# Performance work log

Hardware: AMD Instinct MI355X
Metric: run time of the kernel (lower is better)

Reference implementation:

```python
import jax, jax.numpy as jnp
import numpy as np

N, E, G = 100000, 1600000, 64
IN, H, OUT = 128, 64, 16  # hidden/2 = 32
SLOPE = 0.01


def setup_inputs() -> dict:
    key = jax.random.key(0)
    ks = jax.random.split(key, 7)
    features = jax.random.normal(ks[0], (N, IN), dtype=jnp.float32)
    src = jax.random.randint(ks[1], (E,), 0, N)
    dst = jax.random.randint(ks[2], (E,), 0, N)
    graph_ids = jnp.sort(jax.random.randint(ks[3], (N,), 0, G))
    # kaiming-uniform-ish fan_in init, bias=False everywhere
    W1 = jax.random.uniform(ks[4], (IN, H), jnp.float32, -1.0, 1.0) * np.sqrt(3.0 / IN)
    W2 = jax.random.uniform(ks[5], (H, H // 2), jnp.float32, -1.0, 1.0) * np.sqrt(3.0 / H)
    Wc = jax.random.uniform(ks[6], (H // 2, OUT), jnp.float32, -1.0, 1.0) * np.sqrt(3.0 / (H // 2))
    return {"features": features, "src": src, "dst": dst, "graph_ids": graph_ids,
            "W1": W1, "W2": W2, "Wc": Wc}


def _graph_conv(x, W, src, dst, n):
    # DGL GraphConv, norm='both', bias=False:
    # out = D_in^{-1/2} A (D_out^{-1/2} x) W   (degrees clamped to >= 1)
    ones = jnp.ones(src.shape[0], dtype=x.dtype)
    outdeg = jnp.clip(jax.ops.segment_sum(ones, src, num_segments=n), 1.0)
    indeg = jnp.clip(jax.ops.segment_sum(ones, dst, num_segments=n), 1.0)
    h = (x * jax.lax.rsqrt(outdeg)[:, None]) @ W  # project first (in_dim > out_dim)
    m = jax.ops.segment_sum(h[src], dst, num_segments=n)  # sparse aggregation
    return m * jax.lax.rsqrt(indeg)[:, None]


def reference(features, src, dst, graph_ids, W1, W2, Wc):
    h = jax.nn.leaky_relu(_graph_conv(features, W1, src, dst, N), SLOPE)
    h = jax.nn.leaky_relu(_graph_conv(h, W2, src, dst, N), SLOPE)
    # dropout is identity at inference
    sums = jax.ops.segment_sum(h, graph_ids, num_segments=G)
    cnts = jnp.clip(jax.ops.segment_sum(jnp.ones((N,), h.dtype), graph_ids, num_segments=G), 1.0)
    mean = sums / cnts[:, None]  # dgl.mean_nodes
    return mean @ Wc  # [G, OUT]
```

## Files before the change

### kernel.cpp

```cpp
#include <hip/hip_runtime.h>

#define NN 100000
#define NE 1600000
#define NG 64
#define D_IN 128
#define D_H 64
#define D_H2 32
#define D_OUT 16
#define SLOPE 0.01f
#define REC 48

#define BSH 9
#define NBK 196
#define NCB 500
#define CHE (NE / NCB)
#define PCAP 48

typedef _Float16 half2v __attribute__((ext_vector_type(2)));
typedef _Float16 h8 __attribute__((ext_vector_type(8)));
typedef float f32x4 __attribute__((ext_vector_type(4)));

__global__ __launch_bounds__(512) void p12_scatter(const int* __restrict__ src,
                                                   const int* __restrict__ dst,
                                                   unsigned* __restrict__ pkD,
                                                   unsigned short* __restrict__ pkS,
                                                   int* __restrict__ cntD,
                                                   int* __restrict__ cntS,
                                                   float* __restrict__ pool) {
  __shared__ unsigned stD[NBK][PCAP];
  __shared__ unsigned short stS[NBK][PCAP];
  __shared__ int cD[NBK], cS[NBK];
  int b = blockIdx.x, t = threadIdx.x;
  if (b == 0) {
    for (int i = t; i < NG * D_H2; i += 512) pool[i] = 0.f;
  }
  for (int i = t; i < NBK; i += 512) { cD[i] = 0; cS[i] = 0; }
  __syncthreads();
  const int4* s4 = (const int4*)(src + b * CHE);
  const int4* d4 = (const int4*)(dst + b * CHE);
  for (int i = t; i < CHE / 4; i += 512) {
    int4 s = s4[i], d = d4[i];
#pragma unroll
    for (int j = 0; j < 4; ++j) {
      int ss = (j == 0) ? s.x : (j == 1) ? s.y : (j == 2) ? s.z : s.w;
      int dd = (j == 0) ? d.x : (j == 1) ? d.y : (j == 2) ? d.z : d.w;
      int kd = dd >> BSH;
      int pd = atomicAdd(&cD[kd], 1);
      if (pd < PCAP) stD[kd][pd] = ((unsigned)(dd & 511) << 17) | (unsigned)ss;
      int ks = ss >> BSH;
      int ps = atomicAdd(&cS[ks], 1);
      if (ps < PCAP) stS[ks][ps] = (unsigned short)(ss & 511);
    }
  }
  __syncthreads();
  int wid = t >> 6, lane = t & 63;
  for (int k = wid; k < NBK; k += 8) {
    int cd = min(cD[k], PCAP), cs = min(cS[k], PCAP);
    if (lane < cd) pkD[((size_t)k * NCB + b) * PCAP + lane] = stD[k][lane];
    if (lane < cs) pkS[((size_t)k * NCB + b) * PCAP + lane] = stS[k][lane];
  }
  for (int i = t; i < NBK; i += 512) {
    cntD[i * NCB + b] = min(cD[i], PCAP);
    cntS[i * NCB + b] = min(cS[i], PCAP);
  }
}

__global__ __launch_bounds__(512) void p3_build(const unsigned* __restrict__ pkD,
                                                const unsigned short* __restrict__ pkS,
                                                const int* __restrict__ cntD,
                                                const int* __restrict__ cntS,
                                                int* __restrict__ adj,
                                                int* __restrict__ indeg,
                                                int* __restrict__ outdeg) {
  __shared__ int hh[512];
  int bb = blockIdx.x, t = threadIdx.x;
  hh[t] = 0;
  __syncthreads();
  if (bb < NBK) {
    int k = bb;
    int n0 = k << BSH;
    if (t < NCB) {
      int cnt = cntD[k * NCB + t];
      const uint4* r4 = (const uint4*)(pkD + ((size_t)k * NCB + t) * PCAP);
      for (int i = 0; i * 4 < cnt; ++i) {
        uint4 v = r4[i];
#pragma unroll
        for (int j = 0; j < 4; ++j) {
          int idx = i * 4 + j;
          if (idx < cnt) {
            unsigned rec = (j == 0) ? v.x : (j == 1) ? v.y : (j == 2) ? v.z : v.w;
            int local = rec >> 17;
            int pos = atomicAdd(&hh[local], 1);
            if (pos < REC) adj[(size_t)(n0 + local) * REC + pos] = (int)(rec & 0x1FFFF);
          }
        }
      }
    }
    __syncthreads();
    int n = n0 + t;
    if (n < NN) indeg[n] = hh[t];
  } else {
    int k = bb - NBK;
    if (t < NCB) {
      int cnt = cntS[k * NCB + t];
      const uint4* r4 = (const uint4*)(pkS + ((size_t)k * NCB + t) * PCAP);
      for (int i = 0; i * 8 < cnt; ++i) {
        uint4 v = r4[i];
        const unsigned short* u = (const unsigned short*)&v;
#pragma unroll
        for (int j = 0; j < 8; ++j) {
          int idx = i * 8 + j;
          if (idx < cnt) atomicAdd(&hh[u[j]], 1);
        }
      }
    }
    __syncthreads();
    int n0 = k << BSH;
    int n = n0 + t;
    if (n < NN) outdeg[n] = hh[t];
  }
}

__global__ __launch_bounds__(256) void k_mm1f(const float* __restrict__ X,
                                              const float* __restrict__ W,
                                              const int* __restrict__ odeg,
                                              _Float16* __restrict__ Y) {
  __shared__ _Float16 Wt[64][136];
  int t = threadIdx.x;
  if (blockIdx.x == 0 && t < 64) Y[(size_t)NN * 64 + t] = (_Float16)0.f;
  for (int i = t; i < 128 * 64; i += 256) {
    int k = i >> 6, f = i & 63;
    Wt[f][k] = (_Float16)W[i];
  }
  __syncthreads();
  int lane = t & 63, w = t >> 6;
  int m = lane & 15, q = lane >> 4;
  h8 bf[4][4];
#pragma unroll
  for (int kc = 0; kc < 4; ++kc)
#pragma unroll
    for (int nt = 0; nt < 4; ++nt)
      bf[kc][nt] = *(const h8*)&Wt[nt * 16 + m][kc * 32 + q * 8];

  const int NT = NN / 16;
  int idx = blockIdx.x * 4 + w;
  int t0 = idx * 2, t1 = t0 + 1;
  f32x4 r0[8], r1[8];
  if (t0 < NT) {
    const f32x4* X0 = (const f32x4*)(X + (size_t)(t0 * 16 + m) * 128);
#pragma unroll
    for (int kc = 0; kc < 4; ++kc) {
      r0[kc * 2 + 0] = X0[kc * 8 + q * 2 + 0];
      r0[kc * 2 + 1] = X0[kc * 8 + q * 2 + 1];
    }
  }
  if (t1 < NT) {
    const f32x4* X1 = (const f32x4*)(X + (size_t)(t1 * 16 + m) * 128);
#pragma unroll
    for (int kc = 0; kc < 4; ++kc) {
      r1[kc * 2 + 0] = X1[kc * 8 + q * 2 + 0];
      r1[kc * 2 + 1] = X1[kc * 8 + q * 2 + 1];
    }
  }
#pragma unroll
  for (int half = 0; half < 2; ++half) {
    int tile = (half == 0) ? t0 : t1;
    if (tile >= NT) continue;
    f32x4* rr = (half == 0) ? r0 : r1;
    f32x4 acc[4] = {{0,0,0,0},{0,0,0,0},{0,0,0,0},{0,0,0,0}};
#pragma unroll
    for (int kc = 0; kc < 4; ++kc) {
      f32x4 x0 = rr[kc * 2 + 0], x1 = rr[kc * 2 + 1];
      h8 a;
      a[0] = (_Float16)x0.x; a[1] = (_Float16)x0.y;
      a[2] = (_Float16)x0.z; a[3] = (_Float16)x0.w;
      a[4] = (_Float16)x1.x; a[5] = (_Float16)x1.y;
      a[6] = (_Float16)x1.z; a[7] = (_Float16)x1.w;
#pragma unroll
      for (int nt = 0; nt < 4; ++nt)
        acc[nt] = __builtin_amdgcn_mfma_f32_16x16x32_f16(a, bf[kc][nt], acc[nt], 0, 0, 0);
    }
    int n0 = tile * 16;
#pragma unroll
    for (int reg = 0; reg < 4; ++reg) {
      int nn = n0 + q * 4 + reg;
      float sc = rsqrtf((float)max(odeg[nn], 1));
#pragma unroll
      for (int nt = 0; nt < 4; ++nt)
        Y[(size_t)nn * 64 + nt * 16 + m] = (_Float16)(acc[nt][reg] * sc);
    }
  }
}

__global__ __launch_bounds__(128)
void k_aggmm2(const int* __restrict__ adj,
              const int* __restrict__ indeg,
              const int* __restrict__ odeg,
              const h8* __restrict__ H8,
              const float* __restrict__ W,
              _Float16* __restrict__ Y) {
  __shared__ int Adj[16][REC];
  __shared__ int Deg[16];
  __shared__ _Float16 Ht[16][72];
  __shared__ _Float16 Wt[32][72];
  int t = threadIdx.x;
  if (blockIdx.x == 0 && t < 32) Y[(size_t)NN * 32 + t] = (_Float16)0.f;
  for (int i = t; i < 64 * 32; i += 128) {
    int k = i >> 5, f = i & 31;
    Wt[f][k] = (_Float16)W[i];
  }
  int node0 = blockIdx.x * 16;
  {
    const int4* gadj = (const int4*)(adj + (size_t)node0 * REC);
    for (int i = t; i < 16 * (REC / 4); i += 128)
      ((int4*)Adj)[i] = gadj[i];
    if (t < 16) Deg[t] = indeg[node0 + t];
  }
  __syncthreads();
  for (int i = t; i < 16 * REC; i += 128) {
    int ndc = i / REC, j = i % REC;
    if (j >= min(Deg[ndc], REC)) Adj[ndc][j] = NN;
  }
  __syncthreads();
  int l8 = t & 7;
  int nd = t >> 3;
  int deg = Deg[nd];
  int groups = (min(deg, REC) + 15) >> 4;
  float acc[8] = {0.f, 0.f, 0.f, 0.f, 0.f, 0.f, 0.f, 0.f};
  for (int g = 0; g < groups; ++g) {
    int4 c0 = *(const int4*)&Adj[nd][g * 16 + 0];
    int4 c1 = *(const int4*)&Adj[nd][g * 16 + 4];
    int4 c2 = *(const int4*)&Adj[nd][g * 16 + 8];
    int4 c3 = *(const int4*)&Adj[nd][g * 16 + 12];
    h8 v0 = H8[(size_t)c0.x * 8 + l8];
    h8 v1 = H8[(size_t)c0.y * 8 + l8];
    h8 v2 = H8[(size_t)c0.z * 8 + l8];
    h8 v3 = H8[(size_t)c0.w * 8 + l8];
    h8 v4 = H8[(size_t)c1.x * 8 + l8];
    h8 v5 = H8[(size_t)c1.y * 8 + l8];
    h8 v6 = H8[(size_t)c1.z * 8 + l8];
    h8 v7 = H8[(size_t)c1.w * 8 + l8];
    h8 v8 = H8[(size_t)c2.x * 8 + l8];
    h8 v9 = H8[(size_t)c2.y * 8 + l8];
    h8 va = H8[(size_t)c2.z * 8 + l8];
    h8 vb = H8[(size_t)c2.w * 8 + l8];
    h8 vc = H8[(size_t)c3.x * 8 + l8];
    h8 vd = H8[(size_t)c3.y * 8 + l8];
    h8 ve = H8[(size_t)c3.z * 8 + l8];
    h8 vf = H8[(size_t)c3.w * 8 + l8];
#pragma unroll
    for (int j = 0; j < 8; ++j)
      acc[j] += ((((float)v0[j] + (float)v1[j]) + ((float)v2[j] + (float)v3[j])) +
                 (((float)v4[j] + (float)v5[j]) + ((float)v6[j] + (float)v7[j]))) +
                ((((float)v8[j] + (float)v9[j]) + ((float)va[j] + (float)vb[j])) +
                 (((float)vc[j] + (float)vd[j]) + ((float)ve[j] + (float)vf[j])));
  }
  float sc = rsqrtf((float)max(deg, 1));
  h8 hv;
#pragma unroll
  for (int j = 0; j < 8; ++j) {
    float x = acc[j] * sc;
    hv[j] = (_Float16)((x > 0.f) ? x : SLOPE * x);
  }
  *(h8*)&Ht[nd][l8 * 8] = hv;
  __syncthreads();
  int lane = t & 63, w = t >> 6;
  int m = lane & 15, q = lane >> 4;
  h8 bf[2], af[2];
#pragma unroll
  for (int kc = 0; kc < 2; ++kc) {
    bf[kc] = *(const h8*)&Wt[w * 16 + m][kc * 32 + q * 8];
    af[kc] = *(const h8*)&Ht[m][kc * 32 + q * 8];
  }
  f32x4 acc2 = {0, 0, 0, 0};
#pragma unroll
  for (int kc = 0; kc < 2; ++kc)
    acc2 = __builtin_amdgcn_mfma_f32_16x16x32_f16(af[kc], bf[kc], acc2, 0, 0, 0);
#pragma unroll
  for (int reg = 0; reg < 4; ++reg) {
    int nn = node0 + q * 4 + reg;
    float sco = rsqrtf((float)max(odeg[nn], 1));
    Y[(size_t)nn * 32 + w * 16 + m] = (_Float16)(acc2[reg] * sco);
  }
}

__global__ __launch_bounds__(128)
void k_agg32p(const int* __restrict__ adj,
              const int* __restrict__ indeg,
              const int* __restrict__ gid,
              const h8* __restrict__ H8,
              float* __restrict__ pool) {
  __shared__ int Adj2[32][REC];
  __shared__ int Deg2[32];
  __shared__ float lp[4][D_H2];
  __shared__ int gmin_s;
  int t = threadIdx.x;
  int l4 = t & 3;
  int nd = t >> 2;
  int node0 = blockIdx.x * 32;
  int node = node0 + nd;
  if (t == 0) gmin_s = gid[node0];
  if (t < 4 * D_H2) ((float*)lp)[t] = 0.f;
  {
    const int4* gadj = (const int4*)(adj + (size_t)node0 * REC);
    for (int i = t; i < 32 * (REC / 4); i += 128)
      ((int4*)Adj2)[i] = gadj[i];
    if (t < 32) Deg2[t] = indeg[node0 + t];
  }
  __syncthreads();
  for (int i = t; i < 32 * REC; i += 128) {
    int ndc = i / REC, j = i % REC;
    if (j >= min(Deg2[ndc], REC)) Adj2[ndc][j] = NN;
  }
  __syncthreads();
  int deg = Deg2[nd];
  int groups = (min(deg, REC) + 15) >> 4;
  float acc[8] = {0.f, 0.f, 0.f, 0.f, 0.f, 0.f, 0.f, 0.f};
  for (int g = 0; g < groups; ++g) {
    int4 c0 = *(const int4*)&Adj2[nd][g * 16 + 0];
    int4 c1 = *(const int4*)&Adj2[nd][g * 16 + 4];
    int4 c2 = *(const int4*)&Adj2[nd][g * 16 + 8];
    int4 c3 = *(const int4*)&Adj2[nd][g * 16 + 12];
    h8 v0 = H8[(size_t)c0.x * 4 + l4];
    h8 v1 = H8[(size_t)c0.y * 4 + l4];
    h8 v2 = H8[(size_t)c0.z * 4 + l4];
    h8 v3 = H8[(size_t)c0.w * 4 + l4];
    h8 v4 = H8[(size_t)c1.x * 4 + l4];
    h8 v5 = H8[(size_t)c1.y * 4 + l4];
    h8 v6 = H8[(size_t)c1.z * 4 + l4];
    h8 v7 = H8[(size_t)c1.w * 4 + l4];
    h8 v8 = H8[(size_t)c2.x * 4 + l4];
    h8 v9 = H8[(size_t)c2.y * 4 + l4];
    h8 va = H8[(size_t)c2.z * 4 + l4];
    h8 vb = H8[(size_t)c2.w * 4 + l4];
    h8 vc = H8[(size_t)c3.x * 4 + l4];
    h8 vd = H8[(size_t)c3.y * 4 + l4];
    h8 ve = H8[(size_t)c3.z * 4 + l4];
    h8 vf = H8[(size_t)c3.w * 4 + l4];
#pragma unroll
    for (int j = 0; j < 8; ++j)
      acc[j] += ((((float)v0[j] + (float)v1[j]) + ((float)v2[j] + (float)v3[j])) +
                 (((float)v4[j] + (float)v5[j]) + ((float)v6[j] + (float)v7[j]))) +
                ((((float)v8[j] + (float)v9[j]) + ((float)va[j] + (float)vb[j])) +
                 (((float)vc[j] + (float)vd[j]) + ((float)ve[j] + (float)vf[j])));
  }
  {
    float sc = rsqrtf((float)max(deg, 1));
    int gl = min(gid[node] - gmin_s, 3);
#pragma unroll
    for (int j = 0; j < 8; ++j) {
      float x = acc[j] * sc;
      x = (x > 0.f) ? x : SLOPE * x;
      atomicAdd(&lp[gl][l4 * 8 + j], x);
    }
  }
  __syncthreads();
  {
    float v = ((float*)lp)[t];
    if (v != 0.f) {
      int gl = t >> 5, f = t & 31;
      atomicAdd(&pool[(gmin_s + gl) * D_H2 + f], v);
    }
  }
}

__global__ __launch_bounds__(256) void k_out(const float* __restrict__ pool,
                                             const int* __restrict__ gid,
                                             const float* __restrict__ Wc,
                                             float* __restrict__ out) {
  __shared__ int bnd[NG + 1];
  __shared__ float mean[NG][D_H2];
  int t = threadIdx.x;
  if (t <= NG) {
    int target = t;
    int lo = 0, hi = NN;
    while (lo < hi) {
      int mid = (lo + hi) >> 1;
      if (gid[mid] < target) lo = mid + 1; else hi = mid;
    }
    bnd[t] = lo;
  }
  __syncthreads();
  for (int i = t; i < NG * D_H2; i += 256) {
    int g = i >> 5;
    float inv = 1.0f / (float)max(bnd[g + 1] - bnd[g], 1);
    ((float*)mean)[i] = pool[i] * inv;
  }
  __syncthreads();
  for (int i = t; i < NG * D_OUT; i += 256) {
    int g = i / D_OUT, o = i % D_OUT;
    float s = 0.f;
#pragma unroll
    for (int c = 0; c < D_H2; ++c) s += mean[g][c] * Wc[c * D_OUT + o];
    out[i] = s;
  }
}

extern "C" void kernel_launch(void* const* d_in, const int* in_sizes, int n_in,
                              void* d_out, int out_size, void* d_ws, size_t ws_size,
                              hipStream_t stream) {
  const float* X  = (const float*)d_in[0];
  const int*   src = (const int*)d_in[1];
  const int*   dst = (const int*)d_in[2];
  const int*   gid = (const int*)d_in[3];
  const float* W1 = (const float*)d_in[4];
  const float* W2 = (const float*)d_in[5];
  const float* Wc = (const float*)d_in[6];
  float* out = (float*)d_out;

  char* p = (char*)d_ws;
  auto alloc = [&](size_t bytes) {
    char* q = p;
    p += (bytes + 255) & ~(size_t)255;
    return q;
  };
  float*          pool   = (float*)alloc(NG * D_H2 * 4);
  int*            outdeg = (int*)alloc(NN * 4);
  int*            indeg  = (int*)alloc(NN * 4);
  int*            cntD   = (int*)alloc((size_t)NBK * NCB * 4);
  int*            cntS   = (int*)alloc((size_t)NBK * NCB * 4);
  unsigned*       pkD    = (unsigned*)alloc((size_t)NBK * NCB * PCAP * 4);
  unsigned short* pkS    = (unsigned short*)alloc((size_t)NBK * NCB * PCAP * 2);
  int*            adj    = (int*)alloc((size_t)NN * REC * 4);
  _Float16*       bufA   = (_Float16*)alloc((size_t)(NN + 1) * 64 * 2);
  _Float16*       bufC   = (_Float16*)alloc((size_t)(NN + 1) * 32 * 2);

  p12_scatter<<<NCB, 512, 0, stream>>>(src, dst, pkD, pkS, cntD, cntS, pool);
  p3_build<<<2 * NBK, 512, 0, stream>>>(pkD, pkS, cntD, cntS, adj, indeg, outdeg);

  k_mm1f<<<782, 256, 0, stream>>>(X, W1, outdeg, bufA);
  k_aggmm2<<<NN / 16, 128, 0, stream>>>(adj, indeg, outdeg, (const h8*)bufA, W2, bufC);
  k_agg32p<<<NN / 32, 128, 0, stream>>>(adj, indeg, gid, (const h8*)bufC, pool);
  k_out<<<1, 256, 0, stream>>>(pool, gid, Wc, out);
}
```

Baseline: 206.5 us.

## Fuse final readout into last pooling block and pad adjacency per node

The separate single-block output kernel is folded into the pooling-aggregation kernel: each block increments a global counter after its pool atomics, and the last block to finish computes graph means and the final projection, saving one launch. The adjacency padding with sentinel indices is now done only up to the next multiple of 16 by the threads owning each node, which drops a full-array pass and a barrier in both aggregation kernels. Shared memory is reused between the aggregation and readout phases. The last-block pattern adds a threadfence and a global atomic per block.

After: 345.4 us. +67.3%, slower.

```diff
diff --git a/kernel.cpp b/kernel.cpp
--- a/kernel.cpp
+++ b/kernel.cpp
@@ -26,13 +26,15 @@
                                                    unsigned short* __restrict__ pkS,
                                                    int* __restrict__ cntD,
                                                    int* __restrict__ cntS,
-                                                   float* __restrict__ pool) {
+                                                   float* __restrict__ pool,
+                                                   int* __restrict__ done) {
   __shared__ unsigned stD[NBK][PCAP];
   __shared__ unsigned short stS[NBK][PCAP];
   __shared__ int cD[NBK], cS[NBK];
   int b = blockIdx.x, t = threadIdx.x;
   if (b == 0) {
     for (int i = t; i < NG * D_H2; i += 512) pool[i] = 0.f;
+    if (t == 0) done[0] = 0;
   }
   for (int i = t; i < NBK; i += 512) { cD[i] = 0; cS[i] = 0; }
   __syncthreads();
@@ -217,14 +219,14 @@
     if (t < 16) Deg[t] = indeg[node0 + t];
   }
   __syncthreads();
-  for (int i = t; i < 16 * REC; i += 128) {
-    int ndc = i / REC, j = i % REC;
-    if (j >= min(Deg[ndc], REC)) Adj[ndc][j] = NN;
-  }
-  __syncthreads();
   int l8 = t & 7;
   int nd = t >> 3;
   int deg = Deg[nd];
+  {
+    int dg = min(deg, REC);
+    int dr = min((dg + 15) & ~15, REC);
+    for (int j = dg + l8; j < dr; j += 8) Adj[nd][j] = NN;
+  }
   int groups = (min(deg, REC) + 15) >> 4;
   float acc[8] = {0.f, 0.f, 0.f, 0.f, 0.f, 0.f, 0.f, 0.f};
   for (int g = 0; g < groups; ++g) {
@@ -289,18 +291,25 @@
               const int* __restrict__ indeg,
               const int* __restrict__ gid,
               const h8* __restrict__ H8,
-              float* __restrict__ pool) {
-  __shared__ int Adj2[32][REC];
-  __shared__ int Deg2[32];
-  __shared__ float lp[4][D_H2];
-  __shared__ int gmin_s;
+              float* __restrict__ pool,
+              int* __restrict__ done,
+              const float* __restrict__ Wc,
+              float* __restrict__ out) {
+  __shared__ __align__(16) char smem[8576];
+  int*   Adj2 = (int*)smem;
+  int*   Deg2 = (int*)(smem + 6144);
+  float* lp   = (float*)(smem + 6272);
+  int*   gmsp = (int*)(smem + 6784);
+  float* mean = (float*)smem;
+  int*   bnd  = (int*)(smem + 8192);
+  __shared__ int lastflag;
   int t = threadIdx.x;
   int l4 = t & 3;
   int nd = t >> 2;
   int node0 = blockIdx.x * 32;
   int node = node0 + nd;
-  if (t == 0) gmin_s = gid[node0];
-  if (t < 4 * D_H2) ((float*)lp)[t] = 0.f;
+  if (t == 0) *gmsp = gid[node0];
+  if (t < 4 * D_H2) lp[t] = 0.f;
   {
     const int4* gadj = (const int4*)(adj + (size_t)node0 * REC);
     for (int i = t; i < 32 * (REC / 4); i += 128)
@@ -308,19 +317,20 @@
     if (t < 32) Deg2[t] = indeg[node0 + t];
   }
   __syncthreads();
-  for (int i = t; i < 32 * REC; i += 128) {
-    int ndc = i / REC, j = i % REC;
-    if (j >= min(Deg2[ndc], REC)) Adj2[ndc][j] = NN;
-  }
-  __syncthreads();
+  int gmin = *gmsp;
   int deg = Deg2[nd];
+  {
+    int dg = min(deg, REC);
+    int dr = min((dg + 15) & ~15, REC);
+    for (int j = dg + l4; j < dr; j += 4) Adj2[nd * REC + j] = NN;
+  }
   int groups = (min(deg, REC) + 15) >> 4;
   float acc[8] = {0.f, 0.f, 0.f, 0.f, 0.f, 0.f, 0.f, 0.f};
   for (int g = 0; g < groups; ++g) {
-    int4 c0 = *(const int4*)&Adj2[nd][g * 16 + 0];
-    int4 c1 = *(const int4*)&Adj2[nd][g * 16 + 4];
-    int4 c2 = *(const int4*)&Adj2[nd][g * 16 + 8];
-    int4 c3 = *(const int4*)&Adj2[nd][g * 16 + 12];
+    int4 c0 = *(const int4*)&Adj2[nd * REC + g * 16 + 0];
+    int4 c1 = *(const int4*)&Adj2[nd * REC + g * 16 + 4];
+    int4 c2 = *(const int4*)&Adj2[nd * REC + g * 16 + 8];
+    int4 c3 = *(const int4*)&Adj2[nd * REC + g * 16 + 12];
     h8 v0 = H8[(size_t)c0.x * 4 + l4];
     h8 v1 = H8[(size_t)c0.y * 4 + l4];
     h8 v2 = H8[(size_t)c0.z * 4 + l4];
@@ -346,31 +356,26 @@
   }
   {
     float sc = rsqrtf((float)max(deg, 1));
-    int gl = min(gid[node] - gmin_s, 3);
+    int gl = min(gid[node] - gmin, 3);
 #pragma unroll
     for (int j = 0; j < 8; ++j) {
       float x = acc[j] * sc;
       x = (x > 0.f) ? x : SLOPE * x;
-      atomicAdd(&lp[gl][l4 * 8 + j], x);
-    }
-  }
-  __syncthreads();
-  {
-    float v = ((float*)lp)[t];
+      atomicAdd(&lp[gl * D_H2 + l4 * 8 + j], x);
+    }
+  }
+  __syncthreads();
+  {
+    float v = lp[t];
     if (v != 0.f) {
       int gl = t >> 5, f = t & 31;
-      atomicAdd(&pool[(gmin_s + gl) * D_H2 + f], v);
-    }
-  }
-}
-
-__global__ __launch_bounds__(256) void k_out(const float* __restrict__ pool,
-                                             const int* __restrict__ gid,
-                                             const float* __restrict__ Wc,
-                                             float* __restrict__ out) {
-  __shared__ int bnd[NG + 1];
-  __shared__ float mean[NG][D_H2];
-  int t = threadIdx.x;
+      atomicAdd(&pool[(gmin + gl) * D_H2 + f], v);
+    }
+  }
+  __threadfence();
+  if (t == 0) lastflag = (atomicAdd(done, 1) == (NN / 32) - 1) ? 1 : 0;
+  __syncthreads();
+  if (!lastflag) return;
   if (t <= NG) {
     int target = t;
     int lo = 0, hi = NN;
@@ -381,17 +386,18 @@
     bnd[t] = lo;
   }
   __syncthreads();
-  for (int i = t; i < NG * D_H2; i += 256) {
+  for (int i = t; i < NG * D_H2; i += 128) {
     int g = i >> 5;
     float inv = 1.0f / (float)max(bnd[g + 1] - bnd[g], 1);
-    ((float*)mean)[i] = pool[i] * inv;
-  }
-  __syncthreads();
-  for (int i = t; i < NG * D_OUT; i += 256) {
+    float pv = __hip_atomic_load(&pool[i], __ATOMIC_RELAXED, __HIP_MEMORY_SCOPE_AGENT);
+    mean[i] = pv * inv;
+  }
+  __syncthreads();
+  for (int i = t; i < NG * D_OUT; i += 128) {
     int g = i / D_OUT, o = i % D_OUT;
     float s = 0.f;
 #pragma unroll
-    for (int c = 0; c < D_H2; ++c) s += mean[g][c] * Wc[c * D_OUT + o];
+    for (int c = 0; c < D_H2; ++c) s += mean[g * D_H2 + c] * Wc[c * D_OUT + o];
     out[i] = s;
   }
 }
@@ -415,6 +421,7 @@
     return q;
   };
   float*          pool   = (float*)alloc(NG * D_H2 * 4);
+  int*            done   = (int*)alloc(256);
   int*            outdeg = (int*)alloc(NN * 4);
   int*            indeg  = (int*)alloc(NN * 4);
   int*            cntD   = (int*)alloc((size_t)NBK * NCB * 4);
@@ -425,11 +432,11 @@
   _Float16*       bufA   = (_Float16*)alloc((size_t)(NN + 1) * 64 * 2);
   _Float16*       bufC   = (_Float16*)alloc((size_t)(NN + 1) * 32 * 2);
 
-  p12_scatter<<<NCB, 512, 0, stream>>>(src, dst, pkD, pkS, cntD, cntS, pool);
+  p12_scatter<<<NCB, 512, 0, stream>>>(src, dst, pkD, pkS, cntD, cntS, pool, done);
   p3_build<<<2 * NBK, 512, 0, stream>>>(pkD, pkS, cntD, cntS, adj, indeg, outdeg);
 
   k_mm1f<<<782, 256, 0, stream>>>(X, W1, outdeg, bufA);
   k_aggmm2<<<NN / 16, 128, 0, stream>>>(adj, indeg, outdeg, (const h8*)bufA, W2, bufC);
-  k_agg32p<<<NN / 32, 128, 0, stream>>>(adj, indeg, gid, (const h8*)bufC, pool);
-  k_out<<<1, 256, 0, stream>>>(pool, gid, Wc, out);
-}
+  k_agg32p<<<NN / 32, 128, 0, stream>>>(adj, indeg, gid, (const h8*)bufC, pool,
+                                        done, Wc, out);
+}
```
